# Optimization experiments

Measured on AMD Instinct MI355X. Metric: run time of the kernel, lower is better.

The kernel has to match this reference:

```python
import jax, jax.numpy as jnp
import numpy as np

N, E, F_IN, HID, OUT, B = 8192, 262144, 128, 256, 128, 64


def setup_inputs() -> dict:
    key = jax.random.key(0)
    ks = jax.random.split(key, 8)
    node_features = jax.random.normal(ks[0], (N, F_IN), dtype=jnp.float32)
    edge_index = jax.random.randint(ks[1], (2, E), 0, N, dtype=jnp.int64)
    batch = jnp.sort(jax.random.randint(ks[2], (N,), 0, B, dtype=jnp.int64))
    # GCN layer params (nn.Linear: y = x @ W + b)
    W1 = jax.random.normal(ks[3], (F_IN, HID), dtype=jnp.float32) / np.sqrt(F_IN)
    b1 = jax.random.normal(ks[4], (HID,), dtype=jnp.float32) * 0.01
    W2 = jax.random.normal(ks[5], (HID, OUT), dtype=jnp.float32) / np.sqrt(HID)
    b2 = jax.random.normal(ks[6], (OUT,), dtype=jnp.float32) * 0.01
    return {
        "node_features": node_features,
        "W1": W1, "b1": b1, "W2": W2, "b2": b2,
        "edge_index": edge_index,
        "batch": batch,
        "num_graphs": B,
    }


def _normalized_adjacency(edge_index, num_nodes, dtype):
    src, dst = edge_index[0], edge_index[1]
    A = jnp.zeros((num_nodes, num_nodes), dtype=dtype)
    A = A.at[src, dst].set(1.0).at[dst, src].set(1.0)  # undirected, set (dedups)
    A = A + jnp.eye(num_nodes, dtype=dtype)            # self-loops
    deg = A.sum(axis=1)
    dis = jnp.where(deg > 0, jax.lax.rsqrt(jnp.where(deg > 0, deg, 1.0)), 0.0)
    return dis[:, None] * A * dis[None, :]


def reference(node_features, W1, b1, W2, b2, edge_index, batch, num_graphs):
    n = node_features.shape[0]
    adj = _normalized_adjacency(edge_index, n, node_features.dtype)
    h = jax.nn.relu(adj @ (node_features @ W1 + b1))  # (N, HID)
    h = adj @ (h @ W2 + b2)                            # (N, OUT)
    # mean pooling per graph
    summed = jax.ops.segment_sum(h, batch, num_segments=num_graphs)
    counts = jax.ops.segment_sum(jnp.ones((n,), h.dtype), batch, num_segments=num_graphs)
    return summed / jnp.maximum(counts, 1.0)[:, None]
```

## Files before the change

kernel.cpp:

```cpp
#include <hip/hip_runtime.h>
#include <hip/hip_bf16.h>

#define N_NODES 8192
#define N_EDGES 262144
#define F_INDIM 128
#define HID 256
#define F_OUT 128
#define N_GRAPHS 64
#define WPR (N_NODES / 32)
#define CAP 160
#define NQ 32

struct alignas(8) bf4 { __hip_bfloat16 a, b, c, d; };

__device__ inline float2 bf2unpack(unsigned int u) {
    float2 r;
    r.x = __uint_as_float(u << 16);
    r.y = __uint_as_float(u & 0xffff0000u);
    return r;
}

__global__ __launch_bounds__(256) void cast_zero(const float* __restrict__ X,
                                                 __hip_bfloat16* __restrict__ Xh,
                                                 unsigned int* __restrict__ mask) {
    int b = blockIdx.x, t = threadIdx.x;
    if (b < 1024) {
        int i = b * 256 + t;
        float4 v = ((const float4*)X)[i];
        bf4 o;
        o.a = __float2bfloat16(v.x); o.b = __float2bfloat16(v.y);
        o.c = __float2bfloat16(v.z); o.d = __float2bfloat16(v.w);
        ((bf4*)Xh)[i] = o;
    } else {
        int i = (b - 1024) * 256 + t;
        uint4 z = {0u, 0u, 0u, 0u};
        ((uint4*)mask)[i] = z;
    }
}

__global__ __launch_bounds__(256) void scatter_edges(const int* __restrict__ ei,
                                                     unsigned int* __restrict__ mask) {
    int e = blockIdx.x * blockDim.x + threadIdx.x;
    if (e >= N_EDGES) return;
    int s = ei[e];
    int d = ei[N_EDGES + e];
    if ((unsigned)s >= N_NODES || (unsigned)d >= N_NODES) return;
    atomicOr(&mask[(size_t)s * WPR + (d >> 5)], 1u << (d & 31));
    atomicOr(&mask[(size_t)d * WPR + (s >> 5)], 1u << (s & 31));
}

__global__ __launch_bounds__(256) void compute_dis(const unsigned int* __restrict__ mask,
                                                   float* __restrict__ dis) {
    int row = (blockIdx.x * blockDim.x + threadIdx.x) >> 6;
    int lane = threadIdx.x & 63;
    uint4 v = ((const uint4*)(mask + (size_t)row * WPR))[lane];
    int c = __popc(v.x) + __popc(v.y) + __popc(v.z) + __popc(v.w);
    for (int off = 32; off; off >>= 1) c += __shfl_down(c, off);
    if (lane == 0) dis[row] = rsqrtf((float)(c + 1));
}

__global__ __launch_bounds__(256) void spmm_scan(const unsigned int* __restrict__ mask,
                                                 const __hip_bfloat16* __restrict__ Xh,
                                                 const float* __restrict__ dis,
                                                 const int* __restrict__ batch,
                                                 float* __restrict__ G,
                                                 float* __restrict__ sv,
                                                 float* __restrict__ u) {
    int w = threadIdx.x >> 6, lane = threadIdx.x & 63;
    int i = blockIdx.x * 4 + w;
    __shared__ int nb[4][CAP];
    __shared__ float nbd[4][CAP];
    __shared__ float ul[4][64];
    ul[w][lane] = 0.0f;
    uint4 v = ((const uint4*)(mask + (size_t)i * WPR))[lane];
    int cnt = __popc(v.x) + __popc(v.y) + __popc(v.z) + __popc(v.w);
    int scan = cnt;
    for (int off = 1; off < 64; off <<= 1) {
        int n = __shfl_up(scan, off);
        if (lane >= off) scan += n;
    }
    int tot = __shfl(scan, 63);
    int idx = scan - cnt;
    int wbase = lane << 7;
    unsigned int wd;
    wd = v.x; while (wd) { int b = __ffs(wd) - 1; wd &= wd - 1; if (idx < CAP) nb[w][idx] = wbase + b;      ++idx; }
    wd = v.y; while (wd) { int b = __ffs(wd) - 1; wd &= wd - 1; if (idx < CAP) nb[w][idx] = wbase + 32 + b; ++idx; }
    wd = v.z; while (wd) { int b = __ffs(wd) - 1; wd &= wd - 1; if (idx < CAP) nb[w][idx] = wbase + 64 + b; ++idx; }
    wd = v.w; while (wd) { int b = __ffs(wd) - 1; wd &= wd - 1; if (idx < CAP) nb[w][idx] = wbase + 96 + b; ++idx; }
    int d = tot; if (d > CAP) d = CAP;
    __syncthreads();
    const unsigned int* Xu = (const unsigned int*)Xh;
    float p = 0.0f;
    for (int t = lane; t < d; t += 64) {
        int j = nb[w][t];
        float dj = dis[j];
        nbd[w][t] = dj;
        p += dj;
        atomicAdd(&ul[w][batch[j] & 63], dj);
    }
    for (int off = 32; off; off >>= 1) p += __shfl_down(p, off);
    float di = dis[i];
    if (lane == 0) {
        sv[i] = di * (di + p);
        atomicAdd(&ul[w][batch[i] & 63], di);
    }
    __syncthreads();
    float2 xi = bf2unpack(Xu[(size_t)i * 64 + lane]);
    float2 a0 = {di * xi.x, di * xi.y};
    float2 a1 = {0,0}, a2 = {0,0}, a3 = {0,0}, a4 = {0,0}, a5 = {0,0}, a6 = {0,0}, a7 = {0,0};
    int k = 0;
    for (; k + 8 <= d; k += 8) {
#define GATH(Q, ACC) { int j = nb[w][k+Q]; float dj = nbd[w][k+Q]; \
        float2 f = bf2unpack(Xu[(size_t)j * 64 + lane]); \
        ACC.x += dj * f.x; ACC.y += dj * f.y; }
        GATH(0, a0) GATH(1, a1) GATH(2, a2) GATH(3, a3)
        GATH(4, a4) GATH(5, a5) GATH(6, a6) GATH(7, a7)
    }
    for (; k < d; ++k) GATH(0, a0)
#undef GATH
    float2 s;
    s.x = ((a0.x + a1.x) + (a2.x + a3.x)) + ((a4.x + a5.x) + (a6.x + a7.x));
    s.y = ((a0.y + a1.y) + (a2.y + a3.y)) + ((a4.y + a5.y) + (a6.y + a7.y));
    float2 o = {di * s.x, di * s.y};
    ((float2*)(G + (size_t)i * F_INDIM))[lane] = o;
    u[(size_t)i * N_GRAPHS + lane] = ul[w][lane];
}

__global__ __launch_bounds__(256) void fused_gemm(const float* __restrict__ G,
                                                  const float* __restrict__ W1,
                                                  const float* __restrict__ b1,
                                                  const float* __restrict__ sv,
                                                  const float* __restrict__ W2,
                                                  const float* __restrict__ b2,
                                                  const float* __restrict__ dis,
                                                  __hip_bfloat16* __restrict__ M2ph,
                                                  float* __restrict__ out) {
    int i0 = blockIdx.x * 16;
    int t = threadIdx.x;
    if (blockIdx.x == 0) {
        float4 z = {0,0,0,0};
        for (int v = t; v < N_GRAPHS * F_OUT / 4; v += 256) ((float4*)out)[v] = z;
    }
    __shared__ float xs[16][F_INDIM];
    __shared__ float hs[16][HID];
    for (int v = t; v < 16 * F_INDIM / 4; v += 256) {
        int r = v >> 5, c4 = (v & 31) << 2;
        *(float4*)&xs[r][c4] = *(const float4*)&G[(size_t)(i0 + r) * F_INDIM + c4];
    }
    __syncthreads();
    {
        int tc = t & 63, tr = t >> 6;
        float4 acc0 = {0,0,0,0}, acc1 = {0,0,0,0}, acc2 = {0,0,0,0}, acc3 = {0,0,0,0};
        const float* wp = W1 + 4 * tc;
        for (int k = 0; k < F_INDIM; k += 4) {
            float4 w0 = *(const float4*)&wp[(size_t)(k + 0) * HID];
            float4 w1 = *(const float4*)&wp[(size_t)(k + 1) * HID];
            float4 w2 = *(const float4*)&wp[(size_t)(k + 2) * HID];
            float4 w3 = *(const float4*)&wp[(size_t)(k + 3) * HID];
#define ROW(R, ACC) { \
            float4 g4 = *(const float4*)&xs[4 * tr + R][k]; \
            ACC.x += g4.x*w0.x; ACC.y += g4.x*w0.y; ACC.z += g4.x*w0.z; ACC.w += g4.x*w0.w; \
            ACC.x += g4.y*w1.x; ACC.y += g4.y*w1.y; ACC.z += g4.y*w1.z; ACC.w += g4.y*w1.w; \
            ACC.x += g4.z*w2.x; ACC.y += g4.z*w2.y; ACC.z += g4.z*w2.z; ACC.w += g4.z*w2.w; \
            ACC.x += g4.w*w3.x; ACC.y += g4.w*w3.y; ACC.z += g4.w*w3.z; ACC.w += g4.w*w3.w; }
            ROW(0, acc0) ROW(1, acc1) ROW(2, acc2) ROW(3, acc3)
#undef ROW
        }
        float4 b = *(const float4*)&b1[4 * tc];
#define EPI(R, ACC) { \
            int r = 4 * tr + R; float s = sv[i0 + r]; float4 res = ACC; \
            hs[r][4 * tc + 0] = fmaxf(res.x + s * b.x, 0.f); \
            hs[r][4 * tc + 1] = fmaxf(res.y + s * b.y, 0.f); \
            hs[r][4 * tc + 2] = fmaxf(res.z + s * b.z, 0.f); \
            hs[r][4 * tc + 3] = fmaxf(res.w + s * b.w, 0.f); }
        EPI(0, acc0) EPI(1, acc1) EPI(2, acc2) EPI(3, acc3)
#undef EPI
    }
    __syncthreads();
    {
        int tc = t & 31, tr = t >> 5;
        float4 acc0 = {0,0,0,0}, acc1 = {0,0,0,0};
        const float* wp = W2 + 4 * tc;
        for (int k = 0; k < HID; k += 4) {
            float4 w0 = *(const float4*)&wp[(size_t)(k + 0) * F_OUT];
            float4 w1 = *(const float4*)&wp[(size_t)(k + 1) * F_OUT];
            float4 w2 = *(const float4*)&wp[(size_t)(k + 2) * F_OUT];
            float4 w3 = *(const float4*)&wp[(size_t)(k + 3) * F_OUT];
#define ROW(R, ACC) { \
            float4 g4 = *(const float4*)&hs[2 * tr + R][k]; \
            ACC.x += g4.x*w0.x; ACC.y += g4.x*w0.y; ACC.z += g4.x*w0.z; ACC.w += g4.x*w0.w; \
            ACC.x += g4.y*w1.x; ACC.y += g4.y*w1.y; ACC.z += g4.y*w1.z; ACC.w += g4.y*w1.w; \
            ACC.x += g4.z*w2.x; ACC.y += g4.z*w2.y; ACC.z += g4.z*w2.z; ACC.w += g4.z*w2.w; \
            ACC.x += g4.w*w3.x; ACC.y += g4.w*w3.y; ACC.z += g4.w*w3.z; ACC.w += g4.w*w3.w; }
            ROW(0, acc0) ROW(1, acc1)
#undef ROW
        }
        float4 b = *(const float4*)&b2[4 * tc];
#define EPI(R, ACC) { \
            int i = i0 + 2 * tr + R; float dd = dis[i]; float4 res = ACC; \
            bf4 o; o.a = __float2bfloat16(dd * (res.x + b.x)); o.b = __float2bfloat16(dd * (res.y + b.y)); \
            o.c = __float2bfloat16(dd * (res.z + b.z)); o.d = __float2bfloat16(dd * (res.w + b.w)); \
            *(bf4*)(M2ph + (size_t)i * F_OUT + 4 * tc) = o; }
        EPI(0, acc0) EPI(1, acc1)
#undef EPI
    }
}

__global__ __launch_bounds__(128) void wpool(const float* __restrict__ u,
                                             const __hip_bfloat16* __restrict__ M2ph,
                                             const int* __restrict__ batch,
                                             float* __restrict__ out) {
    int g = blockIdx.x, q = blockIdx.y, c = threadIdx.x;
    int j0 = q * (N_NODES / NQ);
    const unsigned short* Mu = (const unsigned short*)M2ph;
    __shared__ float us[N_NODES / NQ];
    us[c]       = u[(size_t)(j0 + c) * N_GRAPHS + g];
    us[c + 128] = u[(size_t)(j0 + c + 128) * N_GRAPHS + g];
    __syncthreads();
    float a0 = 0.f, a1 = 0.f, a2 = 0.f, a3 = 0.f, a4 = 0.f, a5 = 0.f, a6 = 0.f, a7 = 0.f;
    for (int jj = 0; jj < N_NODES / NQ; jj += 8) {
#define TERM(Q, ACC) ACC += us[jj + Q] * __uint_as_float((unsigned)Mu[(size_t)(j0 + jj + Q) * F_OUT + c] << 16);
        TERM(0, a0) TERM(1, a1) TERM(2, a2) TERM(3, a3)
        TERM(4, a4) TERM(5, a5) TERM(6, a6) TERM(7, a7)
#undef TERM
    }
    float s = ((a0 + a1) + (a2 + a3)) + ((a4 + a5) + (a6 + a7));
    int lo = 0, hi = N_NODES;
    while (lo < hi) { int m = (lo + hi) >> 1; if (batch[m] < g) lo = m + 1; else hi = m; }
    int start = lo;
    hi = N_NODES;
    while (lo < hi) { int m = (lo + hi) >> 1; if (batch[m] < g + 1) lo = m + 1; else hi = m; }
    int cnt = lo - start;
    atomicAdd(&out[(size_t)g * F_OUT + c], s / (float)(cnt > 0 ? cnt : 1));
}

extern "C" void kernel_launch(void* const* d_in, const int* in_sizes, int n_in,
                              void* d_out, int out_size, void* d_ws, size_t ws_size,
                              hipStream_t stream) {
    const float* X  = (const float*)d_in[0];
    const float* W1 = (const float*)d_in[1];
    const float* b1 = (const float*)d_in[2];
    const float* W2 = (const float*)d_in[3];
    const float* b2 = (const float*)d_in[4];
    const int* ei    = (const int*)d_in[5];
    const int* batch = (const int*)d_in[6];
    float* out = (float*)d_out;

    char* ws = (char*)d_ws;
    unsigned int* mask   = (unsigned int*)(ws);
    __hip_bfloat16* M2ph = (__hip_bfloat16*)(ws + 2097152);
    float* G   = (float*)(ws + 8388608);
    __hip_bfloat16* Xh = (__hip_bfloat16*)(ws + 12582912);
    float* u   = (float*)(ws + 14680064);
    float* dis = (float*)(ws + 30441472);
    float* sv  = (float*)(ws + 30474240);

    cast_zero<<<3072, 256, 0, stream>>>(X, Xh, mask);
    scatter_edges<<<N_EDGES / 256, 256, 0, stream>>>(ei, mask);
    compute_dis<<<N_NODES / 4, 256, 0, stream>>>(mask, dis);
    spmm_scan<<<N_NODES / 4, 256, 0, stream>>>(mask, Xh, dis, batch, G, sv, u);
    fused_gemm<<<N_NODES / 16, 256, 0, stream>>>(G, W1, b1, sv, W2, b2, dis, M2ph, out);
    wpool<<<dim3(N_GRAPHS, NQ), 128, 0, stream>>>(u, M2ph, batch, out);
}
```

Measured before the change: 154.4 us.

## Split each node's neighbor gather across two waves and vectorize edge loads

The SpMM kernel now assigns two wavefronts to each node. One builds the neighbor list, then both waves split the neighbor range for degree weighting and the bf16 feature gather. Partial sums are combined through shared memory. The edge scatter kernel now loads two edges per thread with int2 loads and launches half as many blocks. The goal is more memory-level parallelism in the latency-bound gather, at the cost of extra barriers, an idle wave during list construction, and twice as many blocks.

Result: slower. 158.7 us (+2.8%).

```diff
diff --git a/kernel.cpp b/kernel.cpp
--- a/kernel.cpp
+++ b/kernel.cpp
@@ -40,13 +40,17 @@
 
 __global__ __launch_bounds__(256) void scatter_edges(const int* __restrict__ ei,
                                                      unsigned int* __restrict__ mask) {
-    int e = blockIdx.x * blockDim.x + threadIdx.x;
-    if (e >= N_EDGES) return;
-    int s = ei[e];
-    int d = ei[N_EDGES + e];
-    if ((unsigned)s >= N_NODES || (unsigned)d >= N_NODES) return;
-    atomicOr(&mask[(size_t)s * WPR + (d >> 5)], 1u << (d & 31));
-    atomicOr(&mask[(size_t)d * WPR + (s >> 5)], 1u << (s & 31));
+    int e2 = blockIdx.x * 256 + threadIdx.x;
+    int2 s2 = ((const int2*)ei)[e2];
+    int2 d2 = ((const int2*)(ei + N_EDGES))[e2];
+    if ((unsigned)s2.x < N_NODES && (unsigned)d2.x < N_NODES) {
+        atomicOr(&mask[(size_t)s2.x * WPR + (d2.x >> 5)], 1u << (d2.x & 31));
+        atomicOr(&mask[(size_t)d2.x * WPR + (s2.x >> 5)], 1u << (s2.x & 31));
+    }
+    if ((unsigned)s2.y < N_NODES && (unsigned)d2.y < N_NODES) {
+        atomicOr(&mask[(size_t)s2.y * WPR + (d2.y >> 5)], 1u << (d2.y & 31));
+        atomicOr(&mask[(size_t)d2.y * WPR + (s2.y >> 5)], 1u << (s2.y & 31));
+    }
 }
 
 __global__ __launch_bounds__(256) void compute_dis(const unsigned int* __restrict__ mask,
@@ -59,71 +63,91 @@
     if (lane == 0) dis[row] = rsqrtf((float)(c + 1));
 }
 
-__global__ __launch_bounds__(256) void spmm_scan(const unsigned int* __restrict__ mask,
-                                                 const __hip_bfloat16* __restrict__ Xh,
-                                                 const float* __restrict__ dis,
-                                                 const int* __restrict__ batch,
-                                                 float* __restrict__ G,
-                                                 float* __restrict__ sv,
-                                                 float* __restrict__ u) {
+__global__ __launch_bounds__(256) void spmm_scan2(const unsigned int* __restrict__ mask,
+                                                  const __hip_bfloat16* __restrict__ Xh,
+                                                  const float* __restrict__ dis,
+                                                  const int* __restrict__ batch,
+                                                  float* __restrict__ G,
+                                                  float* __restrict__ sv,
+                                                  float* __restrict__ u) {
     int w = threadIdx.x >> 6, lane = threadIdx.x & 63;
-    int i = blockIdx.x * 4 + w;
-    __shared__ int nb[4][CAP];
-    __shared__ float nbd[4][CAP];
-    __shared__ float ul[4][64];
-    ul[w][lane] = 0.0f;
-    uint4 v = ((const uint4*)(mask + (size_t)i * WPR))[lane];
-    int cnt = __popc(v.x) + __popc(v.y) + __popc(v.z) + __popc(v.w);
-    int scan = cnt;
-    for (int off = 1; off < 64; off <<= 1) {
-        int n = __shfl_up(scan, off);
-        if (lane >= off) scan += n;
-    }
-    int tot = __shfl(scan, 63);
-    int idx = scan - cnt;
-    int wbase = lane << 7;
-    unsigned int wd;
-    wd = v.x; while (wd) { int b = __ffs(wd) - 1; wd &= wd - 1; if (idx < CAP) nb[w][idx] = wbase + b;      ++idx; }
-    wd = v.y; while (wd) { int b = __ffs(wd) - 1; wd &= wd - 1; if (idx < CAP) nb[w][idx] = wbase + 32 + b; ++idx; }
-    wd = v.z; while (wd) { int b = __ffs(wd) - 1; wd &= wd - 1; if (idx < CAP) nb[w][idx] = wbase + 64 + b; ++idx; }
-    wd = v.w; while (wd) { int b = __ffs(wd) - 1; wd &= wd - 1; if (idx < CAP) nb[w][idx] = wbase + 96 + b; ++idx; }
-    int d = tot; if (d > CAP) d = CAP;
+    int r = w >> 1;
+    int half = w & 1;
+    int i = blockIdx.x * 2 + r;
+    __shared__ int    nb[2][CAP];
+    __shared__ float  nbd[2][CAP];
+    __shared__ float  ul[2][64];
+    __shared__ int    dsh[2];
+    __shared__ float  psh[2][2];
+    __shared__ float2 gpart[2][64];
+
+    if (half == 1) ul[r][lane] = 0.0f;
+    if (half == 0) {
+        uint4 v = ((const uint4*)(mask + (size_t)i * WPR))[lane];
+        int cnt = __popc(v.x) + __popc(v.y) + __popc(v.z) + __popc(v.w);
+        int scan = cnt;
+        for (int off = 1; off < 64; off <<= 1) {
+            int n = __shfl_up(scan, off);
+            if (lane >= off) scan += n;
+        }
+        int tot = __shfl(scan, 63);
+        int idx = scan - cnt;
+        int wbase = lane << 7;
+        unsigned int wd;
+        wd = v.x; while (wd) { int b = __ffs(wd) - 1; wd &= wd - 1; if (idx < CAP) nb[r][idx] = wbase + b;      ++idx; }
+        wd = v.y; while (wd) { int b = __ffs(wd) - 1; wd &= wd - 1; if (idx < CAP) nb[r][idx] = wbase + 32 + b; ++idx; }
+        wd = v.z; while (wd) { int b = __ffs(wd) - 1; wd &= wd - 1; if (idx < CAP) nb[r][idx] = wbase + 64 + b; ++idx; }
+        wd = v.w; while (wd) { int b = __ffs(wd) - 1; wd &= wd - 1; if (idx < CAP) nb[r][idx] = wbase + 96 + b; ++idx; }
+        if (lane == 0) dsh[r] = (tot > CAP) ? CAP : tot;
+    }
+    __syncthreads();
+    int d  = dsh[r];
+    int d0 = d >> 1;
+    int lo = half ? d0 : 0;
+    int hi = half ? d  : d0;
+    float di = dis[i];
+    float p = 0.0f;
+    for (int t = lo + lane; t < hi; t += 64) {
+        int j = nb[r][t];
+        float dj = dis[j];
+        nbd[r][t] = dj;
+        p += dj;
+        atomicAdd(&ul[r][batch[j] & 63], dj);
+    }
+    if (half == 0 && lane == 0) atomicAdd(&ul[r][batch[i] & 63], di);
+    for (int off = 32; off; off >>= 1) p += __shfl_down(p, off);
+    if (lane == 0) psh[r][half] = p;
     __syncthreads();
     const unsigned int* Xu = (const unsigned int*)Xh;
-    float p = 0.0f;
-    for (int t = lane; t < d; t += 64) {
-        int j = nb[w][t];
-        float dj = dis[j];
-        nbd[w][t] = dj;
-        p += dj;
-        atomicAdd(&ul[w][batch[j] & 63], dj);
-    }
-    for (int off = 32; off; off >>= 1) p += __shfl_down(p, off);
-    float di = dis[i];
-    if (lane == 0) {
-        sv[i] = di * (di + p);
-        atomicAdd(&ul[w][batch[i] & 63], di);
-    }
-    __syncthreads();
-    float2 xi = bf2unpack(Xu[(size_t)i * 64 + lane]);
-    float2 a0 = {di * xi.x, di * xi.y};
-    float2 a1 = {0,0}, a2 = {0,0}, a3 = {0,0}, a4 = {0,0}, a5 = {0,0}, a6 = {0,0}, a7 = {0,0};
-    int k = 0;
-    for (; k + 8 <= d; k += 8) {
-#define GATH(Q, ACC) { int j = nb[w][k+Q]; float dj = nbd[w][k+Q]; \
+    float2 a0 = {0,0}, a1 = {0,0}, a2 = {0,0}, a3 = {0,0},
+           a4 = {0,0}, a5 = {0,0}, a6 = {0,0}, a7 = {0,0};
+    if (half == 0) {
+        float2 xi = bf2unpack(Xu[(size_t)i * 64 + lane]);
+        a0.x = di * xi.x; a0.y = di * xi.y;
+    }
+    int k = lo;
+    for (; k + 8 <= hi; k += 8) {
+#define GATH(Q, ACC) { int j = nb[r][k+Q]; float dj = nbd[r][k+Q]; \
         float2 f = bf2unpack(Xu[(size_t)j * 64 + lane]); \
         ACC.x += dj * f.x; ACC.y += dj * f.y; }
         GATH(0, a0) GATH(1, a1) GATH(2, a2) GATH(3, a3)
         GATH(4, a4) GATH(5, a5) GATH(6, a6) GATH(7, a7)
     }
-    for (; k < d; ++k) GATH(0, a0)
+    for (; k < hi; ++k) GATH(0, a0)
 #undef GATH
     float2 s;
     s.x = ((a0.x + a1.x) + (a2.x + a3.x)) + ((a4.x + a5.x) + (a6.x + a7.x));
     s.y = ((a0.y + a1.y) + (a2.y + a3.y)) + ((a4.y + a5.y) + (a6.y + a7.y));
-    float2 o = {di * s.x, di * s.y};
-    ((float2*)(G + (size_t)i * F_INDIM))[lane] = o;
-    u[(size_t)i * N_GRAPHS + lane] = ul[w][lane];
+    if (half == 1) gpart[r][lane] = s;
+    __syncthreads();
+    if (half == 0) {
+        float2 o = gpart[r][lane];
+        o.x = di * (s.x + o.x);
+        o.y = di * (s.y + o.y);
+        ((float2*)(G + (size_t)i * F_INDIM))[lane] = o;
+        if (lane == 0) sv[i] = di * (di + psh[r][0] + psh[r][1]);
+        u[(size_t)i * N_GRAPHS + lane] = ul[r][lane];
+    }
 }
 
 __global__ __launch_bounds__(256) void fused_gemm(const float* __restrict__ G,
@@ -256,9 +280,9 @@
     float* sv  = (float*)(ws + 30474240);
 
     cast_zero<<<3072, 256, 0, stream>>>(X, Xh, mask);
-    scatter_edges<<<N_EDGES / 256, 256, 0, stream>>>(ei, mask);
+    scatter_edges<<<N_EDGES / 512, 256, 0, stream>>>(ei, mask);
     compute_dis<<<N_NODES / 4, 256, 0, stream>>>(mask, dis);
-    spmm_scan<<<N_NODES / 4, 256, 0, stream>>>(mask, Xh, dis, batch, G, sv, u);
+    spmm_scan2<<<N_NODES / 2, 256, 0, stream>>>(mask, Xh, dis, batch, G, sv, u);
     fused_gemm<<<N_NODES / 16, 256, 0, stream>>>(G, W1, b1, sv, W2, b2, dis, M2ph, out);
     wpool<<<dim3(N_GRAPHS, NQ), 128, 0, stream>>>(u, M2ph, batch, out);
 }
```
